# Optimization experiments

Measured on AMD Instinct MI355X. Metric: run time of the kernel, lower is better.

Reference implementation:

```python
import jax, jax.numpy as jnp
import numpy as np

HEADS = 8  # from init_kwargs; head_dim = dim // heads is only used as the softmax scale


def setup_inputs() -> dict:
    key = jax.random.key(0)
    k1, k2, k3, k4 = jax.random.split(key, 4)
    B, S, D = 16, 512, 256
    r1, r2 = 3, 16  # TT ranks: rank = [1, 3, 16, 1]
    x = jax.random.normal(k1, (B, S, D), jnp.float32)
    # TT factors of the stacked (3, D, D) QKV weight: (1,3,r1), (r1,D,r2), (r2,D,1)
    ar = jax.random.normal(k2, (1, 3, r1), jnp.float32) * 0.2
    br = jax.random.normal(k3, (r1, D, r2), jnp.float32) * 0.2
    cr = jax.random.normal(k4, (r2, D, 1), jnp.float32) * 0.2
    return {"x": x, "ar": ar, "br": br, "cr": cr}


def reference(x, ar, br, cr):
    B, S, D = x.shape
    r1 = ar.shape[2]           # == 3 (required by the final reshape in the torch code)
    r2 = cr.shape[0]
    Bp = B // r2               # grouped batch after split_heads
    head_dim = D // HEADS

    # df = stack([x,x,x]) -> (3,B,S,D), then view as (3, Bp, r2, S, D)
    x_r = x.reshape(Bp, r2, S, D)
    df5 = jnp.broadcast_to(x_r, (3, Bp, r2, S, D))  # no copy under XLA

    # matmul(df.permute(3,1,2,4,0), ar): contract the stack axis (k) with ar[0]
    t1 = jnp.einsum('kbqsd,ki->sbqdi', df5, ar[0])          # (S, Bp, r2, D, r1)

    # matmul(t1.permute(0,1,4,3,2), br.permute(0,2,1)): contract r2 (q) axis
    scores = jnp.einsum('sbqdi,ieq->sbide', t1, br)         # (S, Bp, r1, D, D)
    scores = scores / jnp.sqrt(jnp.float32(head_dim))
    attn = jax.nn.softmax(scores, axis=-1)                  # softmax over last D

    # matmul(attn, cr.permute(2,1,0)) then permute(2,1,4,0,3)
    out = jnp.einsum('sbide,qe->ibqsd', attn, cr[:, :, 0])  # (r1, Bp, r2, S, D)

    # reshape to (3, B, S, D) (valid since r1 == 3), sum over the stack axis
    out = out.reshape(3, B, S, D).sum(axis=0)               # (B, S, D)
    return out
```

## Files before the change

kernel.cpp:

```cpp
#include <hip/hip_runtime.h>
#include <hip/hip_bf16.h>
#include <math.h>


#define SS 512
#define DD 256
#define R2 16
#define NI 3

#define BR_USH (NI * 8 * 512)
#define CR_USH (16 * 512)
#define WS_USH (BR_USH + CR_USH)

typedef __attribute__((ext_vector_type(8))) short bf16x8;
typedef __attribute__((ext_vector_type(8))) unsigned short ushort8;
typedef __attribute__((ext_vector_type(16))) float f32x16;
typedef __attribute__((ext_vector_type(2))) unsigned uint2v;

union B8 { unsigned w[4]; bf16x8 v; };

static __device__ __forceinline__ unsigned short bf16bits(float f) {
    union { __hip_bfloat16 h; unsigned short u; } c;
    c.h = __float2bfloat16(f);
    return c.u;
}
static __device__ __forceinline__ unsigned packb(float a, float b) {
    union { __hip_bfloat162 h; unsigned u; } c;
    c.h = __float22bfloat162_rn(make_float2(a, b));
    return c.u;
}

__global__ void tt_prep(const float* __restrict__ ar,
                        const float* __restrict__ br,
                        const float* __restrict__ cr,
                        unsigned short* __restrict__ wsf)
{
    const int t = blockIdx.x * 256 + threadIdx.x;
    float cA2[NI];
#pragma unroll
    for (int i = 0; i < NI; ++i) {
        float A = ar[0 * NI + i] + ar[1 * NI + i] + ar[2 * NI + i];
        cA2[i] = A * (0.17677669529663687f * 1.4426950408889634f);
    }
    if (t < NI * 8 * 64) {
        const int l = t & 63, et = (t >> 6) & 7, i = t >> 9;
        const float* src = br + (i * DD + et * 32 + (l & 31)) * R2 + 8 * (l >> 5);
        const float sc = cA2[i];
        ushort8 v;
#pragma unroll
        for (int j = 0; j < 8; ++j) v[j] = bf16bits(src[j] * sc);
        *(ushort8*)(wsf + t * 8) = v;
    } else {
        const int idx = t - NI * 8 * 64;
        const int l = idx & 63, h = (idx >> 6) & 1, et = idx >> 7;
        const int b = l & 31;
        ushort8 v;
#pragma unroll
        for (int j = 0; j < 8; ++j) {
            const int e = et * 32 + h * 16 + 8 * (l >> 5) + j;
            float val = (b < 16) ? cr[b * DD + e] : (b == 16 ? 1.0f : 0.0f);
            v[j] = bf16bits(val);
        }
        *(ushort8*)(wsf + (BR_USH + idx * 8)) = v;
    }
}

__global__ __launch_bounds__(256, 4) void tt_attn_mfma(
    const float* __restrict__ x,
    const unsigned short* __restrict__ wsf,
    float* __restrict__ out)
{
    __shared__ unsigned short lds[WS_USH];

    const int s     = blockIdx.x >> 1;
    const int dhalf = blockIdx.x & 1;
    const int tid   = threadIdx.x;
    const int lane  = tid & 63;
    const int wv    = tid >> 6;
    const int hi    = lane >> 5;
    const int d     = dhalf * 128 + wv * 32 + (lane & 31);

#pragma unroll
    for (int c = 0; c < 10; ++c) {
        const char* g = (const char*)wsf + (size_t)(c * 256 + tid) * 16;
        char* lp = (char*)lds + (size_t)(c * 256 + wv * 64) * 16;
        __builtin_amdgcn_global_load_lds(
            (const __attribute__((address_space(1))) void*)g,
            (__attribute__((address_space(3))) void*)lp, 16, 0, 0);
    }

    B8 xb;
    const float* xp = x + s * DD + d + (hi ? 8 * SS * DD : 0);
#pragma unroll
    for (int t = 0; t < 4; ++t)
        xb.w[t] = packb(xp[(2 * t) * SS * DD], xp[(2 * t + 1) * SS * DD]);
    const bf16x8 xf = xb.v;

    __syncthreads();

    f32x16 acc0{}, acc1{}, acc2{};
    const f32x16 zf{};

    const unsigned short* brl = lds + lane * 8;
    const unsigned short* crl = lds + BR_USH + lane * 8;

#pragma unroll 2
    for (int et = 0; et < 8; ++et) {
        const bf16x8 crA0 = *(const bf16x8*)(crl + (et * 2 + 0) * 512);
        const bf16x8 crA1 = *(const bf16x8*)(crl + (et * 2 + 1) * 512);
#pragma unroll
        for (int i = 0; i < NI; ++i) {
            const bf16x8 brA = *(const bf16x8*)(brl + (i * 8 + et) * 512);
            f32x16 g = __builtin_amdgcn_mfma_f32_32x32x16_bf16(brA, xf, zf, 0, 0, 0);
            float p[16];
#pragma unroll
            for (int r = 0; r < 16; ++r) p[r] = __builtin_amdgcn_exp2f(g[r]);
            const unsigned w01 = packb(p[0],  p[1]);
            const unsigned w23 = packb(p[2],  p[3]);
            const unsigned w45 = packb(p[4],  p[5]);
            const unsigned w67 = packb(p[6],  p[7]);
            const unsigned w89 = packb(p[8],  p[9]);
            const unsigned wAB = packb(p[10], p[11]);
            const unsigned wCD = packb(p[12], p[13]);
            const unsigned wEF = packb(p[14], p[15]);
            const uint2v s0 = __builtin_amdgcn_permlane32_swap(w01, w45, false, false);
            const uint2v s1 = __builtin_amdgcn_permlane32_swap(w23, w67, false, false);
            const uint2v s2 = __builtin_amdgcn_permlane32_swap(w89, wCD, false, false);
            const uint2v s3 = __builtin_amdgcn_permlane32_swap(wAB, wEF, false, false);
            B8 P0; P0.w[0] = s0.x; P0.w[1] = s1.x; P0.w[2] = s0.y; P0.w[3] = s1.y;
            B8 P1; P1.w[0] = s2.x; P1.w[1] = s3.x; P1.w[2] = s2.y; P1.w[3] = s3.y;
            if (i == 0) {
                acc0 = __builtin_amdgcn_mfma_f32_32x32x16_bf16(crA0, P0.v, acc0, 0, 0, 0);
                acc0 = __builtin_amdgcn_mfma_f32_32x32x16_bf16(crA1, P1.v, acc0, 0, 0, 0);
            } else if (i == 1) {
                acc1 = __builtin_amdgcn_mfma_f32_32x32x16_bf16(crA0, P0.v, acc1, 0, 0, 0);
                acc1 = __builtin_amdgcn_mfma_f32_32x32x16_bf16(crA1, P1.v, acc1, 0, 0, 0);
            } else {
                acc2 = __builtin_amdgcn_mfma_f32_32x32x16_bf16(crA0, P0.v, acc2, 0, 0, 0);
                acc2 = __builtin_amdgcn_mfma_f32_32x32x16_bf16(crA1, P1.v, acc2, 0, 0, 0);
            }
        }
    }

    float inv[NI];
#pragma unroll
    for (int i = 0; i < NI; ++i) {
        union { float f; unsigned u; } c;
        c.f = (i == 0) ? acc0[8] : (i == 1) ? acc1[8] : acc2[8];
        const uint2v r = __builtin_amdgcn_permlane32_swap(c.u, c.u, false, false);
        union { unsigned u; float f; } c2; c2.u = r.x;
        inv[i] = 1.0f / c2.f;
    }

#pragma unroll
    for (int r = 0; r < 8; ++r) {
        const int b = (r & 3) + 8 * (r >> 2) + 4 * hi;
        const float o = acc0[r] * inv[0] + acc1[r] * inv[1] + acc2[r] * inv[2];
        out[(b * SS + s) * DD + d] = o;
    }
}

extern "C" void kernel_launch(void* const* d_in, const int* in_sizes, int n_in,
                              void* d_out, int out_size, void* d_ws, size_t ws_size,
                              hipStream_t stream) {
    const float* x  = (const float*)d_in[0];
    const float* ar = (const float*)d_in[1];
    const float* br = (const float*)d_in[2];
    const float* cr = (const float*)d_in[3];
    float* out = (float*)d_out;

    unsigned short* wsf = (unsigned short*)d_ws;

    hipLaunchKernelGGL(tt_prep, dim3(10), dim3(256), 0, stream, ar, br, cr, wsf);
    hipLaunchKernelGGL(tt_attn_mfma, dim3(SS * 2), dim3(256), 0, stream, x, wsf, out);
}
```

Baseline: 27.65 us.

## Fuse weight prep kernel into attention kernel, building LDS tiles per block

Removes the separate tt_prep launch and has every block convert the br/cr TT factors to scaled bf16 directly into LDS. The x loads are issued before the weight conversion so their latency overlaps with that work. This drops one kernel launch and the dependency between the two kernels. In exchange, all 1024 blocks repeat the conversion and read the fp32 factors from global memory or cache, which adds redundant ALU and load work.

Measured after the change: 30.28 us. +9.5%, slower.

```diff
diff --git a/kernel.cpp b/kernel.cpp
--- a/kernel.cpp
+++ b/kernel.cpp
@@ -8,12 +8,15 @@
 #define R2 16
 #define NI 3
 
-#define BR_USH (NI * 8 * 512)
-#define CR_USH (16 * 512)
-#define WS_USH (BR_USH + CR_USH)
+#define BR_UNITS (NI * 8 * 64)
+#define CR_UNITS (16 * 64)
+#define ALL_UNITS (BR_UNITS + CR_UNITS)
+#define BR_USH (BR_UNITS * 8)
+#define WS_USH (ALL_UNITS * 8)
 
 typedef __attribute__((ext_vector_type(8))) short bf16x8;
 typedef __attribute__((ext_vector_type(8))) unsigned short ushort8;
+typedef __attribute__((ext_vector_type(4))) float float4v;
 typedef __attribute__((ext_vector_type(16))) float f32x16;
 typedef __attribute__((ext_vector_type(2))) unsigned uint2v;
 
@@ -30,44 +33,11 @@
     return c.u;
 }
 
-__global__ void tt_prep(const float* __restrict__ ar,
-                        const float* __restrict__ br,
-                        const float* __restrict__ cr,
-                        unsigned short* __restrict__ wsf)
-{
-    const int t = blockIdx.x * 256 + threadIdx.x;
-    float cA2[NI];
-#pragma unroll
-    for (int i = 0; i < NI; ++i) {
-        float A = ar[0 * NI + i] + ar[1 * NI + i] + ar[2 * NI + i];
-        cA2[i] = A * (0.17677669529663687f * 1.4426950408889634f);
-    }
-    if (t < NI * 8 * 64) {
-        const int l = t & 63, et = (t >> 6) & 7, i = t >> 9;
-        const float* src = br + (i * DD + et * 32 + (l & 31)) * R2 + 8 * (l >> 5);
-        const float sc = cA2[i];
-        ushort8 v;
-#pragma unroll
-        for (int j = 0; j < 8; ++j) v[j] = bf16bits(src[j] * sc);
-        *(ushort8*)(wsf + t * 8) = v;
-    } else {
-        const int idx = t - NI * 8 * 64;
-        const int l = idx & 63, h = (idx >> 6) & 1, et = idx >> 7;
-        const int b = l & 31;
-        ushort8 v;
-#pragma unroll
-        for (int j = 0; j < 8; ++j) {
-            const int e = et * 32 + h * 16 + 8 * (l >> 5) + j;
-            float val = (b < 16) ? cr[b * DD + e] : (b == 16 ? 1.0f : 0.0f);
-            v[j] = bf16bits(val);
-        }
-        *(ushort8*)(wsf + (BR_USH + idx * 8)) = v;
-    }
-}
-
-__global__ __launch_bounds__(256, 4) void tt_attn_mfma(
+__global__ __launch_bounds__(256, 4) void tt_attn_fused(
     const float* __restrict__ x,
-    const unsigned short* __restrict__ wsf,
+    const float* __restrict__ ar,
+    const float* __restrict__ br,
+    const float* __restrict__ cr,
     float* __restrict__ out)
 {
     __shared__ unsigned short lds[WS_USH];
@@ -80,20 +50,48 @@
     const int hi    = lane >> 5;
     const int d     = dhalf * 128 + wv * 32 + (lane & 31);
 
+    const float* xp = x + s * DD + d + (hi ? 8 * SS * DD : 0);
+    float xr[8];
+#pragma unroll
+    for (int t = 0; t < 8; ++t) xr[t] = xp[t * SS * DD];
+
+    float cA2[NI];
+#pragma unroll
+    for (int i = 0; i < NI; ++i)
+        cA2[i] = (ar[i] + ar[NI + i] + ar[2 * NI + i]) *
+                 (0.17677669529663687f * 1.4426950408889634f);
+
 #pragma unroll
     for (int c = 0; c < 10; ++c) {
-        const char* g = (const char*)wsf + (size_t)(c * 256 + tid) * 16;
-        char* lp = (char*)lds + (size_t)(c * 256 + wv * 64) * 16;
-        __builtin_amdgcn_global_load_lds(
-            (const __attribute__((address_space(1))) void*)g,
-            (__attribute__((address_space(3))) void*)lp, 16, 0, 0);
+        const int idx = c * 256 + tid;
+        ushort8 v;
+        if (idx < BR_UNITS) {
+            const int l = idx & 63, et = (idx >> 6) & 7, i = idx >> 9;
+            const float* src = br + (i * DD + et * 32 + (l & 31)) * R2 + 8 * (l >> 5);
+            const float4v a0 = *(const float4v*)src;
+            const float4v a1 = *(const float4v*)(src + 4);
+            const float sc = cA2[i];
+#pragma unroll
+            for (int j = 0; j < 4; ++j) v[j] = bf16bits(a0[j] * sc);
+#pragma unroll
+            for (int j = 0; j < 4; ++j) v[4 + j] = bf16bits(a1[j] * sc);
+        } else {
+            const int k = idx - BR_UNITS;
+            const int l = k & 63, h = (k >> 6) & 1, et = k >> 7;
+            const int b = l & 31;
+#pragma unroll
+            for (int j = 0; j < 8; ++j) {
+                const int e = et * 32 + h * 16 + 8 * (l >> 5) + j;
+                const float val = (b < 16) ? cr[b * DD + e] : (b == 16 ? 1.0f : 0.0f);
+                v[j] = bf16bits(val);
+            }
+        }
+        *(ushort8*)(lds + idx * 8) = v;
     }
 
     B8 xb;
-    const float* xp = x + s * DD + d + (hi ? 8 * SS * DD : 0);
 #pragma unroll
-    for (int t = 0; t < 4; ++t)
-        xb.w[t] = packb(xp[(2 * t) * SS * DD], xp[(2 * t + 1) * SS * DD]);
+    for (int t = 0; t < 4; ++t) xb.w[t] = packb(xr[2 * t], xr[2 * t + 1]);
     const bf16x8 xf = xb.v;
 
     __syncthreads();
@@ -169,8 +167,6 @@
     const float* cr = (const float*)d_in[3];
     float* out = (float*)d_out;
 
-    unsigned short* wsf = (unsigned short*)d_ws;
-
-    hipLaunchKernelGGL(tt_prep, dim3(10), dim3(256), 0, stream, ar, br, cr, wsf);
-    hipLaunchKernelGGL(tt_attn_mfma, dim3(SS * 2), dim3(256), 0, stream, x, wsf, out);
+    hipLaunchKernelGGL(tt_attn_fused, dim3(SS * 2), dim3(256), 0, stream,
+                       x, ar, br, cr, out);
 }
```

## Split the three rank-i chains across separate waves and reduce through LDS

Applied to the files above, without the earlier changes.

Blocks grow from 256 to 768 threads, with threadIdx.y selecting the rank index i. Each wave group now computes one of the three score/exp/output MFMA chains instead of one wave doing all three in sequence. The partial outputs are normalized, written to LDS by groups 1 and 2, and summed by group 0 before the store. This exposes more parallel waves to hide MFMA and exp latency, but it loads x three times, adds an LDS reduction and a second barrier, and could limit occupancy through the larger block size.

Measured after the change: 28.34 us. 2.5% more time.

```diff
diff --git a/kernel.cpp b/kernel.cpp
--- a/kernel.cpp
+++ b/kernel.cpp
@@ -8,13 +8,16 @@
 #define R2 16
 #define NI 3
 
-#define BR_USH (NI * 8 * 512)
-#define CR_USH (16 * 512)
-#define WS_USH (BR_USH + CR_USH)
+#define BR_UNITS (NI * 8 * 64)
+#define CR_UNITS (16 * 64)
+#define ALL_UNITS (BR_UNITS + CR_UNITS)
+#define BR_USH (BR_UNITS * 8)
+#define WS_USH (ALL_UNITS * 8)
 
 typedef __attribute__((ext_vector_type(8))) short bf16x8;
 typedef __attribute__((ext_vector_type(8))) unsigned short ushort8;
 typedef __attribute__((ext_vector_type(16))) float f32x16;
+typedef __attribute__((ext_vector_type(4))) float float4v;
 typedef __attribute__((ext_vector_type(2))) unsigned uint2v;
 
 union B8 { unsigned w[4]; bf16x8 v; };
@@ -42,7 +45,7 @@
         float A = ar[0 * NI + i] + ar[1 * NI + i] + ar[2 * NI + i];
         cA2[i] = A * (0.17677669529663687f * 1.4426950408889634f);
     }
-    if (t < NI * 8 * 64) {
+    if (t < BR_UNITS) {
         const int l = t & 63, et = (t >> 6) & 7, i = t >> 9;
         const float* src = br + (i * DD + et * 32 + (l & 31)) * R2 + 8 * (l >> 5);
         const float sc = cA2[i];
@@ -51,7 +54,7 @@
         for (int j = 0; j < 8; ++j) v[j] = bf16bits(src[j] * sc);
         *(ushort8*)(wsf + t * 8) = v;
     } else {
-        const int idx = t - NI * 8 * 64;
+        const int idx = t - BR_UNITS;
         const int l = idx & 63, h = (idx >> 6) & 1, et = idx >> 7;
         const int b = l & 31;
         ushort8 v;
@@ -65,98 +68,108 @@
     }
 }
 
-__global__ __launch_bounds__(256, 4) void tt_attn_mfma(
+__global__ __launch_bounds__(768, 6) void tt_attn_mfma(
     const float* __restrict__ x,
     const unsigned short* __restrict__ wsf,
     float* __restrict__ out)
 {
-    __shared__ unsigned short lds[WS_USH];
+    __shared__ unsigned short lds_w[WS_USH];
+    __shared__ float lds_p[2][4][64][8];
 
     const int s     = blockIdx.x >> 1;
     const int dhalf = blockIdx.x & 1;
-    const int tid   = threadIdx.x;
-    const int lane  = tid & 63;
-    const int wv    = tid >> 6;
+    const int tx    = threadIdx.x;
+    const int i     = threadIdx.y;
+    const int lane  = tx & 63;
+    const int wv    = tx >> 6;
     const int hi    = lane >> 5;
     const int d     = dhalf * 128 + wv * 32 + (lane & 31);
+    const int ft    = i * 256 + tx;
 
 #pragma unroll
-    for (int c = 0; c < 10; ++c) {
-        const char* g = (const char*)wsf + (size_t)(c * 256 + tid) * 16;
-        char* lp = (char*)lds + (size_t)(c * 256 + wv * 64) * 16;
-        __builtin_amdgcn_global_load_lds(
-            (const __attribute__((address_space(1))) void*)g,
-            (__attribute__((address_space(3))) void*)lp, 16, 0, 0);
+    for (int c = 0; c < 4; ++c) {
+        const int idx = c * 768 + ft;
+        if (idx < ALL_UNITS) {
+            const char* g = (const char*)wsf + (size_t)idx * 16;
+            char* lp = (char*)lds_w + (size_t)(idx - lane) * 16;
+            __builtin_amdgcn_global_load_lds(
+                (const __attribute__((address_space(1))) void*)g,
+                (__attribute__((address_space(3))) void*)lp, 16, 0, 0);
+        }
     }
 
+    const float* xp = x + s * DD + d + (hi ? 8 * SS * DD : 0);
+    float xr[8];
+#pragma unroll
+    for (int t = 0; t < 8; ++t) xr[t] = xp[t * SS * DD];
     B8 xb;
-    const float* xp = x + s * DD + d + (hi ? 8 * SS * DD : 0);
 #pragma unroll
-    for (int t = 0; t < 4; ++t)
-        xb.w[t] = packb(xp[(2 * t) * SS * DD], xp[(2 * t + 1) * SS * DD]);
+    for (int t = 0; t < 4; ++t) xb.w[t] = packb(xr[2 * t], xr[2 * t + 1]);
     const bf16x8 xf = xb.v;
 
     __syncthreads();
 
-    f32x16 acc0{}, acc1{}, acc2{};
+    f32x16 acc{};
     const f32x16 zf{};
 
-    const unsigned short* brl = lds + lane * 8;
-    const unsigned short* crl = lds + BR_USH + lane * 8;
+    const unsigned short* brl = lds_w + lane * 8;
+    const unsigned short* crl = lds_w + BR_USH + lane * 8;
 
 #pragma unroll 2
     for (int et = 0; et < 8; ++et) {
         const bf16x8 crA0 = *(const bf16x8*)(crl + (et * 2 + 0) * 512);
         const bf16x8 crA1 = *(const bf16x8*)(crl + (et * 2 + 1) * 512);
+        const bf16x8 brA  = *(const bf16x8*)(brl + (i * 8 + et) * 512);
+        f32x16 g = __builtin_amdgcn_mfma_f32_32x32x16_bf16(brA, xf, zf, 0, 0, 0);
+        float p[16];
 #pragma unroll
-        for (int i = 0; i < NI; ++i) {
-            const bf16x8 brA = *(const bf16x8*)(brl + (i * 8 + et) * 512);
-            f32x16 g = __builtin_amdgcn_mfma_f32_32x32x16_bf16(brA, xf, zf, 0, 0, 0);
-            float p[16];
-#pragma unroll
-            for (int r = 0; r < 16; ++r) p[r] = __builtin_amdgcn_exp2f(g[r]);
-            const unsigned w01 = packb(p[0],  p[1]);
-            const unsigned w23 = packb(p[2],  p[3]);
-            const unsigned w45 = packb(p[4],  p[5]);
-            const unsigned w67 = packb(p[6],  p[7]);
-            const unsigned w89 = packb(p[8],  p[9]);
-            const unsigned wAB = packb(p[10], p[11]);
-            const unsigned wCD = packb(p[12], p[13]);
-            const unsigned wEF = packb(p[14], p[15]);
-            const uint2v s0 = __builtin_amdgcn_permlane32_swap(w01, w45, false, false);
-            const uint2v s1 = __builtin_amdgcn_permlane32_swap(w23, w67, false, false);
-            const uint2v s2 = __builtin_amdgcn_permlane32_swap(w89, wCD, false, false);
-            const uint2v s3 = __builtin_amdgcn_permlane32_swap(wAB, wEF, false, false);
-            B8 P0; P0.w[0] = s0.x; P0.w[1] = s1.x; P0.w[2] = s0.y; P0.w[3] = s1.y;
-            B8 P1; P1.w[0] = s2.x; P1.w[1] = s3.x; P1.w[2] = s2.y; P1.w[3] = s3.y;
-            if (i == 0) {
-                acc0 = __builtin_amdgcn_mfma_f32_32x32x16_bf16(crA0, P0.v, acc0, 0, 0, 0);
-                acc0 = __builtin_amdgcn_mfma_f32_32x32x16_bf16(crA1, P1.v, acc0, 0, 0, 0);
-            } else if (i == 1) {
-                acc1 = __builtin_amdgcn_mfma_f32_32x32x16_bf16(crA0, P0.v, acc1, 0, 0, 0);
-                acc1 = __builtin_amdgcn_mfma_f32_32x32x16_bf16(crA1, P1.v, acc1, 0, 0, 0);
-            } else {
-                acc2 = __builtin_amdgcn_mfma_f32_32x32x16_bf16(crA0, P0.v, acc2, 0, 0, 0);
-                acc2 = __builtin_amdgcn_mfma_f32_32x32x16_bf16(crA1, P1.v, acc2, 0, 0, 0);
-            }
-        }
+        for (int r = 0; r < 16; ++r) p[r] = __builtin_amdgcn_exp2f(g[r]);
+        const unsigned w01 = packb(p[0],  p[1]);
+        const unsigned w23 = packb(p[2],  p[3]);
+        const unsigned w45 = packb(p[4],  p[5]);
+        const unsigned w67 = packb(p[6],  p[7]);
+        const unsigned w89 = packb(p[8],  p[9]);
+        const unsigned wAB = packb(p[10], p[11]);
+        const unsigned wCD = packb(p[12], p[13]);
+        const unsigned wEF = packb(p[14], p[15]);
+        const uint2v s0 = __builtin_amdgcn_permlane32_swap(w01, w45, false, false);
+        const uint2v s1 = __builtin_amdgcn_permlane32_swap(w23, w67, false, false);
+        const uint2v s2 = __builtin_amdgcn_permlane32_swap(w89, wCD, false, false);
+        const uint2v s3 = __builtin_amdgcn_permlane32_swap(wAB, wEF, false, false);
+        B8 P0; P0.w[0] = s0.x; P0.w[1] = s1.x; P0.w[2] = s0.y; P0.w[3] = s1.y;
+        B8 P1; P1.w[0] = s2.x; P1.w[1] = s3.x; P1.w[2] = s2.y; P1.w[3] = s3.y;
+        acc = __builtin_amdgcn_mfma_f32_32x32x16_bf16(crA0, P0.v, acc, 0, 0, 0);
+        acc = __builtin_amdgcn_mfma_f32_32x32x16_bf16(crA1, P1.v, acc, 0, 0, 0);
     }
 
-    float inv[NI];
-#pragma unroll
-    for (int i = 0; i < NI; ++i) {
+    float inv;
+    {
         union { float f; unsigned u; } c;
-        c.f = (i == 0) ? acc0[8] : (i == 1) ? acc1[8] : acc2[8];
+        c.f = acc[8];
         const uint2v r = __builtin_amdgcn_permlane32_swap(c.u, c.u, false, false);
         union { unsigned u; float f; } c2; c2.u = r.x;
-        inv[i] = 1.0f / c2.f;
+        inv = 1.0f / c2.f;
     }
 
+    float sc[8];
 #pragma unroll
-    for (int r = 0; r < 8; ++r) {
-        const int b = (r & 3) + 8 * (r >> 2) + 4 * hi;
-        const float o = acc0[r] * inv[0] + acc1[r] * inv[1] + acc2[r] * inv[2];
-        out[(b * SS + s) * DD + d] = o;
+    for (int r = 0; r < 8; ++r) sc[r] = acc[r] * inv;
+
+    if (i > 0) {
+        float* pp = &lds_p[i - 1][wv][lane][0];
+        *(float4v*)pp       = *(const float4v*)&sc[0];
+        *(float4v*)(pp + 4) = *(const float4v*)&sc[4];
+    }
+    __syncthreads();
+
+    if (i == 0) {
+        const float* p1 = &lds_p[0][wv][lane][0];
+        const float* p2 = &lds_p[1][wv][lane][0];
+#pragma unroll
+        for (int r = 0; r < 8; ++r) {
+            const int b = (r & 3) + 8 * (r >> 2) + 4 * hi;
+            out[(b * SS + s) * DD + d] = sc[r] + p1[r] + p2[r];
+        }
     }
 }
 
@@ -172,5 +185,6 @@
     unsigned short* wsf = (unsigned short*)d_ws;
 
     hipLaunchKernelGGL(tt_prep, dim3(10), dim3(256), 0, stream, ar, br, cr, wsf);
-    hipLaunchKernelGGL(tt_attn_mfma, dim3(SS * 2), dim3(256), 0, stream, x, wsf, out);
+    hipLaunchKernelGGL(tt_attn_mfma, dim3(SS * 2), dim3(256, NI), 0, stream,
+                       x, wsf, out);
 }
```
